# Kernel optimization log

Measured on AMD Instinct MI355X. Metric: run time of the kernel, lower is better.

## Reference

```python
import jax, jax.numpy as jnp
import numpy as np

B, N = 2048, 1023
N_INTS, N_OPS, N_PASSES = 10, 3, 10
NODE_LIT, NODE_OP = 0, 1


def setup_inputs() -> dict:
    key = jax.random.key(0)
    ks = jax.random.split(key, 6)
    cats = jax.random.randint(ks[0], (B, N), 0, 2, dtype=jnp.int32)
    ops = jax.random.randint(ks[1], (B, N), 0, N_OPS, dtype=jnp.int32)
    lits = jax.random.randint(ks[2], (B, N), 0, N_INTS, dtype=jnp.int32)
    left = jax.random.randint(ks[3], (B, N), 0, N, dtype=jnp.int32)
    right = jax.random.randint(ks[4], (B, N), 0, N, dtype=jnp.int32)
    mask = jnp.ones((B, N), dtype=bool)
    op_table = jax.random.normal(ks[5], (N_OPS, N_INTS, N_INTS, N_INTS), dtype=jnp.float32) * 0.1
    return {"op_table": op_table, "cats": cats, "ops": ops, "lits": lits,
            "left": left, "right": right, "mask": mask}


def _gather_nodes(state, idx):
    # state: (B, N, n_ints); idx: (B, N) -> (B, N, n_ints)
    return jnp.take_along_axis(state, jnp.broadcast_to(idx[:, :, None], state.shape), axis=1)


def _op_step(state, op_table, ops_c, left, right, update_mask):
    left_dist = _gather_nodes(state, left)    # (B, N, n_ints)
    right_dist = _gather_nodes(state, right)  # (B, N, n_ints)
    # Compute logits for all ops, then select per-node op slice (equivalent to
    # gathering op_table[ops] then einsum('bni,bnj,bnijk->bnk'), but avoids the
    # (B,N,10,10,10) materialized gather).
    all_logits = jnp.einsum('bni,bnj,oijk->bnok', left_dist, right_dist, op_table)  # (B,N,n_ops,n_ints)
    node_logits = jnp.take_along_axis(all_logits, ops_c[:, :, None, None], axis=2)[:, :, 0, :]
    op_dist = jax.nn.softmax(node_logits, axis=-1)
    new_state = jnp.where(update_mask[:, :, None], op_dist, state)
    return new_state, node_logits


def reference(op_table, cats, ops, lits, left, right, mask):
    left = jnp.clip(left, 0, N - 1)
    right = jnp.clip(right, 0, N - 1)
    ops_c = jnp.clip(ops, 0, N_OPS - 1)

    # init state: literals -> one-hot, everything else -> zeros
    lit_mask = (cats == NODE_LIT) & mask
    lit_onehot = jax.nn.one_hot(jnp.clip(lits, 0, N_INTS - 1), N_INTS, dtype=op_table.dtype)
    state = jnp.where(lit_mask[:, :, None], lit_onehot, jnp.zeros((), op_table.dtype))

    op_mask = (cats == NODE_OP) & mask
    for _ in range(N_PASSES - 1):
        state, _ = _op_step(state, op_table, ops_c, left, right, op_mask)
    state, node_logits = _op_step(state, op_table, ops_c, left, right, op_mask)

    root_is_lit = (cats[:, 0] == NODE_LIT)[:, None]
    root_logits = jnp.where(root_is_lit, state[:, 0, :] * 10.0, node_logits[:, 0, :])
    return root_logits
```

## Files before the change

kernel.cpp:

```cpp
#include <hip/hip_runtime.h>

#define BB 2048
#define NTH 768
#define NN 1023
#define NI 10
#define NPASS 10
#define DUMMY 1023
#define MAXSLOTS 1072
#define LOG2E 1.44269504f
#define LN2 0.69314718f
#define SBYTES 28672

typedef _Float16 half2v __attribute__((ext_vector_type(2)));
typedef _Float16 half8v __attribute__((ext_vector_type(8)));
typedef __fp16   fp16x2 __attribute__((ext_vector_type(2)));
typedef float    floatx4 __attribute__((ext_vector_type(4)));
typedef unsigned int uint;
typedef unsigned long long ull;

#if __has_builtin(__builtin_amdgcn_exp2f)
#define EXP2(x) __builtin_amdgcn_exp2f(x)
#else
#define EXP2(x) exp2f(x)
#endif
#if __has_builtin(__builtin_amdgcn_rcpf)
#define RCP(x) __builtin_amdgcn_rcpf(x)
#else
#define RCP(x) (1.f / (x))
#endif

static __device__ inline uint pkh(float a, float b) {
#if __has_builtin(__builtin_amdgcn_cvt_pkrtz)
    union { fp16x2 h; uint u; } z;
    z.h = __builtin_amdgcn_cvt_pkrtz(a, b);
    return z.u;
#else
    union { uint u; _Float16 h[2]; } z;
    z.h[0] = (_Float16)a; z.h[1] = (_Float16)b; return z.u;
#endif
}

static __device__ inline half2v h2(uint u) {
    union { uint u; half2v h; } z; z.u = u; return z.h;
}

static __device__ inline bool getmask(const void* mraw, bool mbytes, long idx) {
    return mbytes ? (((const unsigned char*)mraw)[idx] != 0)
                  : (((const int*)mraw)[idx] != 0);
}

__global__ __launch_bounds__(64) void prepack_kernel(const float* __restrict__ op_table,
                                                     uint4* __restrict__ tpk) {
    int lane = threadIdx.x;
    int opq  = blockIdx.x;
    int op = opq / 5, q = opq % 5;
    int col = lane & 15, g = lane >> 4, hi = g >> 1, jh = (g & 1) * 8;
    union { uint4 u; _Float16 h[8]; } z;
    #pragma unroll
    for (int e = 0; e < 8; ++e) {
        int i = 5 * hi + q, j = jh + e;
        float v = 0.f;
        if (col < NI && j < NI) v = op_table[op * 1000 + (i * NI + j) * NI + col] * LOG2E;
        z.h[e] = (_Float16)v;
    }
    tpk[opq * 64 + lane] = z.u;
}

template <int MODE>
__global__ __launch_bounds__(NTH, 6)
void circuit_kernel(const float* __restrict__ op_table,
                    const int* __restrict__ cats,
                    const int* __restrict__ ops,
                    const int* __restrict__ lits,
                    const int* __restrict__ left,
                    const int* __restrict__ right,
                    const void* __restrict__ mask_raw,
                    float* __restrict__ out,
                    const uint4* __restrict__ tpk)
{
    __shared__ __align__(16) uint sS[2 * 7168 + 8];
    __shared__ uint sBkt[MAXSLOTS];
    __shared__ int sCtl[16];

    const int b    = blockIdx.x;
    const int tid  = threadIdx.x;
    const int lane = tid & 63;
    const int wave = tid >> 6;
    const int myOp = wave >> 2;
    const int wl   = wave & 3;
    const int col  = lane & 15;
    const int g    = lane >> 4;
    const int hi   = g >> 1;
    const int jh   = (g & 1) * 8;
    const long rowoff = (long)b * NN;

    const uint mw0 = *(const uint*)mask_raw;
    const bool mbytes = (mw0 == 0x01010101u);

    if (tid < 16) sCtl[tid] = 0;
    if (tid < 8) sS[14336 + tid] = 0;

    const uint selA = hi ? 0x03020302u : 0x01000100u;
    const uint selB = hi ? 0x05040504u : 0x03020302u;

    half8v Tf[5];
    if constexpr (MODE == 1) {
        #pragma unroll
        for (int q = 0; q < 5; ++q) {
            union { uint4 u; half8v h; } z;
            z.u = tpk[(myOp * 5 + q) * 64 + lane];
            Tf[q] = z.h;
        }
    } else {
        #pragma unroll
        for (int q = 0; q < 5; ++q) {
            half8v t_;
            #pragma unroll
            for (int e = 0; e < 8; ++e) {
                int i = 5 * hi + q, j = jh + e;
                float v = 0.f;
                if (col < NI && j < NI)
                    v = op_table[myOp * 1000 + (i * NI + j) * NI + col] * LOG2E;
                t_[e] = (_Float16)v;
            }
            Tf[q] = t_;
        }
    }

    int  myop0 = 3, myop1 = 3;
    uint enc0 = 0, enc1 = 0;
    #define INIT_NODE(N, MYOP, ENC)                                              \
    {                                                                            \
        int n = (N);                                                             \
        uint r[7] = {0, 0, 0, 0, 0, 0, 0};                                       \
        if (n < NN) {                                                            \
            int cat = cats[rowoff + n];                                          \
            bool m = getmask(mask_raw, mbytes, rowoff + n);                      \
            if (cat == 0 && m) {                                                 \
                int lit = min(max(lits[rowoff + n], 0), NI - 1);                 \
                r[lit >> 1] = (lit & 1) ? 0x3C000000u : 0x3C00u;                 \
            } else if (cat == 1 && m) {                                          \
                MYOP = min(max(ops[rowoff + n], 0), 2);                          \
                int lf = min(max(left[rowoff + n], 0), NN - 1);                  \
                int rt = min(max(right[rowoff + n], 0), NN - 1);                 \
                ENC = (uint)n | ((uint)lf << 10) | ((uint)rt << 20);             \
            }                                                                    \
        }                                                                        \
        if (n < 1024) {                                                          \
            _Pragma("unroll")                                                    \
            for (int w = 0; w < 7; ++w) {                                        \
                sS[n * 7 + w] = r[w];                                            \
                sS[7168 + n * 7 + w] = r[w];                                     \
            }                                                                    \
        }                                                                        \
    }
    INIT_NODE(tid, myop0, enc0)
    INIT_NODE(tid + NTH, myop1, enc1)
    __syncthreads();

    {
        ull m00 = __ballot(myop0 == 0), m01 = __ballot(myop0 == 1), m02 = __ballot(myop0 == 2);
        ull m10 = __ballot(myop1 == 0), m11 = __ballot(myop1 == 1), m12 = __ballot(myop1 == 2);
        int c0 = __popcll(m00) + __popcll(m10);
        int c1 = __popcll(m01) + __popcll(m11);
        int c2 = __popcll(m02) + __popcll(m12);
        if (lane == 0) {
            if (c0) atomicAdd(&sCtl[0], c0);
            if (c1) atomicAdd(&sCtl[1], c1);
            if (c2) atomicAdd(&sCtl[2], c2);
        }
    }
    __syncthreads();
    if (tid == 0) {
        int c0 = sCtl[0], c1 = sCtl[1], c2 = sCtl[2];
        int p0 = (c0 + 15) & ~15, p1 = (c1 + 15) & ~15, p2 = (c2 + 15) & ~15;
        sCtl[4] = p0; sCtl[5] = p0 + p1; sCtl[9] = p0 + p1 + p2;
        sCtl[6] = 0; sCtl[7] = p0; sCtl[8] = p0 + p1;
    }
    __syncthreads();
    #define PLACE(MYOP, ENC)                                                     \
    {                                                                            \
        _Pragma("unroll")                                                        \
        for (int o = 0; o < 3; ++o) {                                            \
            ull mm = __ballot((MYOP) == o);                                      \
            if (mm) {                                                            \
                int rsv = 0;                                                     \
                if (lane == 0) rsv = atomicAdd(&sCtl[6 + o], __popcll(mm));      \
                rsv = __shfl(rsv, 0);                                            \
                if ((MYOP) == o)                                                 \
                    sBkt[rsv + __popcll(mm & ((1ull << lane) - 1))] = (ENC);     \
            }                                                                    \
        }                                                                        \
    }
    PLACE(myop0, enc0)
    PLACE(myop1, enc1)
    __syncthreads();
    {
        uint dv = (uint)DUMMY | ((uint)DUMMY << 10) | ((uint)DUMMY << 20);
        int f0 = sCtl[6], e0b = sCtl[4];
        int f1 = sCtl[7], e1b = sCtl[5];
        int f2 = sCtl[8], e2b = sCtl[9];
        if (tid < e0b - f0) sBkt[f0 + tid] = dv;
        if (tid < e1b - f1) sBkt[f1 + tid] = dv;
        if (tid < e2b - f2) sBkt[f2 + tid] = dv;
    }
    __syncthreads();

    const int tB1 = __builtin_amdgcn_readfirstlane(sCtl[4] >> 4);
    const int tB2 = __builtin_amdgcn_readfirstlane(sCtl[5] >> 4);
    const int tB3 = __builtin_amdgcn_readfirstlane(sCtl[9] >> 4);
    const int t_lo = (myOp == 0) ? 0   : ((myOp == 1) ? tB1 : tB2);
    const int t_hi = (myOp == 0) ? tB1 : ((myOp == 1) ? tB2 : tB3);
    const int first = t_lo + wl;
    const int nIter = (t_hi > first) ? ((t_hi - first + 3) >> 2) : 0;
    const int cat0 = cats[rowoff];
    const bool rootActive = (cat0 == 1) && getmask(mask_raw, mbytes, rowoff);

    uint LA0 = 0, RA0 = 0, WA0 = 0, LA1 = 0, RA1 = 0, WA1 = 0, LA2 = 0, RA2 = 0, WA2 = 0;
    bool RT0 = false, RT1 = false, RT2 = false;
    #define CACHE1(K, LA, RA, WA, RT)                                            \
    if (nIter > K) {                                                             \
        uint E = sBkt[(first + K * 4) * 16 + col];                               \
        uint n_ = E & 1023u, lf_ = (E >> 10) & 1023u, rt_ = (E >> 20) & 1023u;   \
        LA = lf_ * 28u + 8u * (uint)hi;                                          \
        RA = rt_ * 28u + 2u * (uint)jh;                                          \
        WA = n_ * 28u + 8u * (uint)g;                                            \
        RT = (n_ == 0u);                                                         \
    }
    CACHE1(0, LA0, RA0, WA0, RT0)
    CACHE1(1, LA1, RA1, WA1, RT1)
    CACHE1(2, LA2, RA2, WA2, RT2)

    char* sbase = (char*)&sS[0];

    #define MSTQ(QI, LU) {                                                       \
        half2v l2v = h2(LU);                                                     \
        union { half8v v8; half2v v2[4]; } au;                                   \
        au.v2[0] = l2v * R0; au.v2[1] = l2v * R1;                                \
        au.v2[2] = l2v * R2; au.v2[3] = l2v * R3;                                \
        C = __builtin_amdgcn_mfma_f32_16x16x32_f16(Tf[QI], au.v8, C, 0, 0, 0);   \
    }
    #define ITER_BODY(LA, RA, WA, RT)                                            \
    {                                                                            \
        const uint* lpd = (const uint*)(rbase + (LA));                           \
        const uint* rp  = (const uint*)(rbase + (RA));                           \
        uint D0 = lpd[0], D1 = lpd[1], D2 = lpd[2];                              \
        half2v R0 = h2(rp[0]), R1 = h2(rp[1]), R2 = h2(rp[2]), R3 = h2(rp[3]);   \
        uint L0, L1, L2, L3, L4;                                                 \
        L0 = __builtin_amdgcn_perm(D0, D0, selA);                                \
        L1 = __builtin_amdgcn_perm(D1, D0, selB);                                \
        L2 = __builtin_amdgcn_perm(D1, D1, selA);                                \
        L3 = __builtin_amdgcn_perm(D2, D1, selB);                                \
        L4 = __builtin_amdgcn_perm(D2, D2, selA);                                \
        floatx4 C = {0.f, 0.f, 0.f, 0.f};                                        \
        MSTQ(0, L0) MSTQ(1, L1) MSTQ(2, L2) MSTQ(3, L3) MSTQ(4, L4)              \
        if (lastp && (RT)) {                                                     \
            if (g < 2) {                                                         \
                out[b * NI + 4 * g + 0] = C[0] * LN2;                            \
                out[b * NI + 4 * g + 1] = C[1] * LN2;                            \
                out[b * NI + 4 * g + 2] = C[2] * LN2;                            \
                out[b * NI + 4 * g + 3] = C[3] * LN2;                            \
            } else if (g == 2) {                                                 \
                out[b * NI + 8] = C[0] * LN2;                                    \
                out[b * NI + 9] = C[1] * LN2;                                    \
            }                                                                    \
        }                                                                        \
        float e0 = 0.f, e1 = 0.f, e2 = 0.f, e3 = 0.f, part;                      \
        if (g < 2) {                                                             \
            e0 = EXP2(C[0]); e1 = EXP2(C[1]); e2 = EXP2(C[2]); e3 = EXP2(C[3]);  \
            part = (e0 + e1) + (e2 + e3);                                        \
        } else if (g == 2) {                                                     \
            e0 = EXP2(C[0]); e1 = EXP2(C[1]); part = e0 + e1;                    \
        } else part = 0.f;                                                       \
        part += __shfl_xor(part, 16);                                            \
        part += __shfl_xor(part, 32);                                            \
        float inv = RCP(part);                                                   \
        if (g < 2) {                                                             \
            uint* wp = (uint*)(wbase + (WA));                                    \
            wp[0] = pkh(e0 * inv, e1 * inv);                                     \
            wp[1] = pkh(e2 * inv, e3 * inv);                                     \
        } else if (g == 2) {                                                     \
            *(uint*)(wbase + (WA)) = pkh(e0 * inv, e1 * inv);                    \
        }                                                                        \
    }

    for (int p = 0; p < NPASS; ++p) {
        const bool lastp = (p == NPASS - 1);
        char* rbase = sbase + ((p & 1) ? SBYTES : 0);
        char* wbase = sbase + ((p & 1) ? 0 : SBYTES);

        if (nIter > 0) ITER_BODY(LA0, RA0, WA0, RT0)
        if (nIter > 1) ITER_BODY(LA1, RA1, WA1, RT1)
        if (nIter > 2) ITER_BODY(LA2, RA2, WA2, RT2)
        for (int it = 3; it < nIter; ++it) {
            uint E = sBkt[(first + it * 4) * 16 + col];
            uint n_ = E & 1023u, lf_ = (E >> 10) & 1023u, rt_ = (E >> 20) & 1023u;
            uint LAx = lf_ * 28u + 8u * (uint)hi;
            uint RAx = rt_ * 28u + 2u * (uint)jh;
            uint WAx = n_ * 28u + 8u * (uint)g;
            bool RTx = (n_ == 0u);
            ITER_BODY(LAx, RAx, WAx, RTx)
        }
        __syncthreads();
    }

    if (cat0 == 1 && !rootActive && tid == 0) {
        int op0 = min(max(ops[rowoff], 0), 2);
        int lf0 = min(max(left[rowoff], 0), NN - 1);
        int rt0 = min(max(right[rowoff], 0), NN - 1);
        const _Float16* sh = (const _Float16*)((char*)sS + SBYTES);
        float acc[NI];
        #pragma unroll
        for (int k = 0; k < NI; ++k) acc[k] = 0.f;
        for (int i = 0; i < NI; ++i) {
            float li = (float)sh[lf0 * 14 + i];
            for (int j = 0; j < NI; ++j) {
                float w = li * (float)sh[rt0 * 14 + j];
                #pragma unroll
                for (int k = 0; k < NI; ++k)
                    acc[k] = fmaf(w, op_table[op0 * 1000 + (i * NI + j) * NI + k], acc[k]);
            }
        }
        #pragma unroll
        for (int k = 0; k < NI; ++k) out[b * NI + k] = acc[k];
    }

    if (cat0 == 0 && tid < NI) {
        out[b * NI + tid] = (float)((const _Float16*)sS)[tid] * 10.f;
    }
}

extern "C" void kernel_launch(void* const* d_in, const int* in_sizes, int n_in,
                              void* d_out, int out_size, void* d_ws, size_t ws_size,
                              hipStream_t stream) {
    const float* op_table = (const float*)d_in[0];
    const int*   cats     = (const int*)d_in[1];
    const int*   ops      = (const int*)d_in[2];
    const int*   lits     = (const int*)d_in[3];
    const int*   left     = (const int*)d_in[4];
    const int*   right    = (const int*)d_in[5];
    const void*  mask     = d_in[6];
    float* out = (float*)d_out;

    const size_t tbytes = (size_t)15 * 64 * sizeof(uint4);

    if (ws_size >= tbytes) {
        uint4* tpk = (uint4*)d_ws;
        prepack_kernel<<<dim3(15), dim3(64), 0, stream>>>(op_table, tpk);
        circuit_kernel<1><<<dim3(BB), dim3(NTH), 0, stream>>>(
            op_table, cats, ops, lits, left, right, mask, out, tpk);
    } else {
        circuit_kernel<0><<<dim3(BB), dim3(NTH), 0, stream>>>(
            op_table, cats, ops, lits, left, right, mask, out, nullptr);
    }
}
```

Before: 139.3 us.

## Balance waves across ops by per-op tile counts instead of fixed split

Instead of giving each of the three ops exactly four of the twelve waves, thread 0 now assigns waves to ops greedily in proportion to each op's tile count. Each wave then strides through its op's tiles by that op's wave count. The goal is to shorten the busiest wave's tile list in every pass, since each pass ends at a block barrier. It also computes exp2 unconditionally to avoid divergence and merges two 32-bit LDS stores into one 64-bit store. The cost is a runtime integer divide for the stride and op-table loading moved after the barrier.

```diff
diff --git a/kernel.cpp b/kernel.cpp
--- a/kernel.cpp
+++ b/kernel.cpp
@@ -2,6 +2,7 @@
 
 #define BB 2048
 #define NTH 768
+#define NWAVE 12
 #define NN 1023
 #define NI 10
 #define NPASS 10
@@ -86,8 +87,6 @@
     const int tid  = threadIdx.x;
     const int lane = tid & 63;
     const int wave = tid >> 6;
-    const int myOp = wave >> 2;
-    const int wl   = wave & 3;
     const int col  = lane & 15;
     const int g    = lane >> 4;
     const int hi   = g >> 1;
@@ -102,30 +101,6 @@
 
     const uint selA = hi ? 0x03020302u : 0x01000100u;
     const uint selB = hi ? 0x05040504u : 0x03020302u;
-
-    half8v Tf[5];
-    if constexpr (MODE == 1) {
-        #pragma unroll
-        for (int q = 0; q < 5; ++q) {
-            union { uint4 u; half8v h; } z;
-            z.u = tpk[(myOp * 5 + q) * 64 + lane];
-            Tf[q] = z.h;
-        }
-    } else {
-        #pragma unroll
-        for (int q = 0; q < 5; ++q) {
-            half8v t_;
-            #pragma unroll
-            for (int e = 0; e < 8; ++e) {
-                int i = 5 * hi + q, j = jh + e;
-                float v = 0.f;
-                if (col < NI && j < NI)
-                    v = op_table[myOp * 1000 + (i * NI + j) * NI + col] * LOG2E;
-                t_[e] = (_Float16)v;
-            }
-            Tf[q] = t_;
-        }
-    }
 
     int  myop0 = 3, myop1 = 3;
     uint enc0 = 0, enc1 = 0;
@@ -176,8 +151,50 @@
         int p0 = (c0 + 15) & ~15, p1 = (c1 + 15) & ~15, p2 = (c2 + 15) & ~15;
         sCtl[4] = p0; sCtl[5] = p0 + p1; sCtl[9] = p0 + p1 + p2;
         sCtl[6] = 0; sCtl[7] = p0; sCtl[8] = p0 + p1;
-    }
-    __syncthreads();
+        int tc0 = p0 >> 4, tc1 = p1 >> 4, tc2 = p2 >> 4;
+        int w0 = 0, w1 = 0, w2 = 0;
+        for (int k = 0; k < NWAVE; ++k) {
+            float pr0 = (w0 == 0) ? ((tc0 > 0) ? 1e9f : -1.f) : (float)tc0 / (float)w0;
+            float pr1 = (w1 == 0) ? ((tc1 > 0) ? 1e9f : -1.f) : (float)tc1 / (float)w1;
+            float pr2 = (w2 == 0) ? ((tc2 > 0) ? 1e9f : -1.f) : (float)tc2 / (float)w2;
+            if (pr0 >= pr1 && pr0 >= pr2) ++w0;
+            else if (pr1 >= pr2) ++w1;
+            else ++w2;
+        }
+        sCtl[10] = w0; sCtl[11] = w0 + w1;
+    }
+    __syncthreads();
+
+    const int W0  = __builtin_amdgcn_readfirstlane(sCtl[10]);
+    const int W01 = __builtin_amdgcn_readfirstlane(sCtl[11]);
+    const int myOp = (wave < W0) ? 0 : ((wave < W01) ? 1 : 2);
+    const int wl   = wave - ((myOp == 0) ? 0 : ((myOp == 1) ? W0 : W01));
+    const int wstride = (myOp == 0) ? W0 : ((myOp == 1) ? (W01 - W0) : (NWAVE - W01));
+
+    half8v Tf[5];
+    if constexpr (MODE == 1) {
+        #pragma unroll
+        for (int q = 0; q < 5; ++q) {
+            union { uint4 u; half8v h; } z;
+            z.u = tpk[(myOp * 5 + q) * 64 + lane];
+            Tf[q] = z.h;
+        }
+    } else {
+        #pragma unroll
+        for (int q = 0; q < 5; ++q) {
+            half8v t_;
+            #pragma unroll
+            for (int e = 0; e < 8; ++e) {
+                int i = 5 * hi + q, j = jh + e;
+                float v = 0.f;
+                if (col < NI && j < NI)
+                    v = op_table[myOp * 1000 + (i * NI + j) * NI + col] * LOG2E;
+                t_[e] = (_Float16)v;
+            }
+            Tf[q] = t_;
+        }
+    }
+
     #define PLACE(MYOP, ENC)                                                     \
     {                                                                            \
         _Pragma("unroll")                                                        \
@@ -212,7 +229,7 @@
     const int t_lo = (myOp == 0) ? 0   : ((myOp == 1) ? tB1 : tB2);
     const int t_hi = (myOp == 0) ? tB1 : ((myOp == 1) ? tB2 : tB3);
     const int first = t_lo + wl;
-    const int nIter = (t_hi > first) ? ((t_hi - first + 3) >> 2) : 0;
+    const int nIter = (t_hi > first) ? ((t_hi - first + wstride - 1) / wstride) : 0;
     const int cat0 = cats[rowoff];
     const bool rootActive = (cat0 == 1) && getmask(mask_raw, mbytes, rowoff);
 
@@ -220,7 +237,7 @@
     bool RT0 = false, RT1 = false, RT2 = false;
     #define CACHE1(K, LA, RA, WA, RT)                                            \
     if (nIter > K) {                                                             \
-        uint E = sBkt[(first + K * 4) * 16 + col];                               \
+        uint E = sBkt[(first + K * wstride) * 16 + col];                         \
         uint n_ = E & 1023u, lf_ = (E >> 10) & 1023u, rt_ = (E >> 20) & 1023u;   \
         LA = lf_ * 28u + 8u * (uint)hi;                                          \
         RA = rt_ * 28u + 2u * (uint)jh;                                          \
@@ -265,20 +282,17 @@
                 out[b * NI + 9] = C[1] * LN2;                                    \
             }                                                                    \
         }                                                                        \
-        float e0 = 0.f, e1 = 0.f, e2 = 0.f, e3 = 0.f, part;                      \
-        if (g < 2) {                                                             \
-            e0 = EXP2(C[0]); e1 = EXP2(C[1]); e2 = EXP2(C[2]); e3 = EXP2(C[3]);  \
-            part = (e0 + e1) + (e2 + e3);                                        \
-        } else if (g == 2) {                                                     \
-            e0 = EXP2(C[0]); e1 = EXP2(C[1]); part = e0 + e1;                    \
-        } else part = 0.f;                                                       \
+        float e0 = EXP2(C[0]), e1 = EXP2(C[1]);                                  \
+        float e2 = EXP2(C[2]), e3 = EXP2(C[3]);                                  \
+        float part = (g < 2) ? ((e0 + e1) + (e2 + e3))                           \
+                             : ((g == 2) ? (e0 + e1) : 0.f);                     \
         part += __shfl_xor(part, 16);                                            \
         part += __shfl_xor(part, 32);                                            \
         float inv = RCP(part);                                                   \
         if (g < 2) {                                                             \
-            uint* wp = (uint*)(wbase + (WA));                                    \
-            wp[0] = pkh(e0 * inv, e1 * inv);                                     \
-            wp[1] = pkh(e2 * inv, e3 * inv);                                     \
+            uint2 w2; w2.x = pkh(e0 * inv, e1 * inv);                            \
+            w2.y = pkh(e2 * inv, e3 * inv);                                      \
+            *(uint2*)(wbase + (WA)) = w2;                                        \
         } else if (g == 2) {                                                     \
             *(uint*)(wbase + (WA)) = pkh(e0 * inv, e1 * inv);                    \
         }                                                                        \
@@ -293,7 +307,7 @@
         if (nIter > 1) ITER_BODY(LA1, RA1, WA1, RT1)
         if (nIter > 2) ITER_BODY(LA2, RA2, WA2, RT2)
         for (int it = 3; it < nIter; ++it) {
-            uint E = sBkt[(first + it * 4) * 16 + col];
+            uint E = sBkt[(first + it * wstride) * 16 + col];
             uint n_ = E & 1023u, lf_ = (E >> 10) & 1023u, rt_ = (E >> 20) & 1023u;
             uint LAx = lf_ * 28u + 8u * (uint)hi;
             uint RAx = rt_ * 28u + 2u * (uint)jh;
```

Result: slower. 150.2 us (+7.9%).
